# Kernel optimization log

Hardware: AMD Instinct MI355X
Metric: run time of the kernel (lower is better)

The kernel has to match this reference:

```python
import jax, jax.numpy as jnp
import numpy as np

S, B, C, H, E, V, T = 196, 64, 1024, 1024, 512, 32000, 20


def setup_inputs() -> dict:
    key = jax.random.key(0)
    ks = jax.random.split(key, 16)

    def w(k, shape, fan_in):
        return (jax.random.normal(k, shape, jnp.float32) / np.sqrt(fan_in)).astype(jnp.float32)

    emb_W = w(ks[2], (V, E), E).at[0].set(0.0)  # padding_idx=0
    return {
        'ctx': jax.random.normal(ks[0], (S, B, C), jnp.float32),
        'y': jax.random.randint(ks[1], (T, B), 0, V, jnp.int32),
        'emb_W': emb_W,
        'att_ctx2ctx': w(ks[3], (C, C), C),
        'att_hid2ctx': w(ks[4], (H, C), H),
        'att_mlp': w(ks[5], (C,), C),
        'gru_W_ih': w(ks[6], (3 * H, E + C), E + C),
        'gru_b_ih': jnp.zeros((3 * H,), jnp.float32),
        'gru_W_hh': w(ks[7], (3 * H, H), H),
        'gru_b_hh': jnp.zeros((3 * H,), jnp.float32),
        'hid2out_W': w(ks[8], (E, H), H),
        'hid2out_b': jnp.zeros((E,), jnp.float32),
        'out_ctx_W': w(ks[9], (E, C), C),
        'out_ctx_b': jnp.zeros((E,), jnp.float32),
        'out2prob_W': w(ks[10], (V, E), E),
        'out2prob_b': jnp.zeros((V,), jnp.float32),
    }


def reference(ctx, y, emb_W, att_ctx2ctx, att_hid2ctx, att_mlp,
              gru_W_ih, gru_b_ih, gru_W_hh, gru_b_hh,
              hid2out_W, hid2out_b, out_ctx_W, out_ctx_b,
              out2prob_W, out2prob_b):
    hidden = gru_W_hh.shape[1]
    y_emb = emb_W[y]                                        # [T, B, E]
    ctx_proj = jnp.einsum('sbc,cm->sbm', ctx, att_ctx2ctx)  # precompute ctx2ctx(ctx)

    def gru_cell(x, h):
        gi = x @ gru_W_ih.T + gru_b_ih
        gh = h @ gru_W_hh.T + gru_b_hh
        i_r, i_z, i_n = jnp.split(gi, 3, axis=-1)
        h_r, h_z, h_n = jnp.split(gh, 3, axis=-1)
        r = jax.nn.sigmoid(i_r + h_r)
        z = jax.nn.sigmoid(i_z + h_z)
        n = jnp.tanh(i_n + r * h_n)
        return (1.0 - z) * n + z * h

    def step(h, inp):
        y_t, tgt = inp                                      # [B,E], [B]
        # MLP attention over source positions S
        scores = jnp.einsum('sbm,m->sb', jnp.tanh(ctx_proj + (h @ att_hid2ctx)[None]), att_mlp)
        alpha = jax.nn.softmax(scores, axis=0)              # [S, B]
        z_t = jnp.einsum('sb,sbc->bc', alpha, ctx)          # [B, C]
        ht = gru_cell(jnp.concatenate([y_t, z_t], axis=-1), h)
        logit = jnp.tanh(ht @ hid2out_W.T + hid2out_b)      # hid2out (tanh FF)
        logit = logit + y_t                                 # prev2out
        logit = logit + z_t @ out_ctx_W.T + out_ctx_b       # ctx2out
        log_p = jax.nn.log_softmax(jnp.tanh(logit) @ out2prob_W.T + out2prob_b, axis=-1)
        mask = (tgt != 0).astype(log_p.dtype)               # NLLLoss ignore_index=0, sum
        nll = -jnp.sum(jnp.take_along_axis(log_p, tgt[:, None], axis=1)[:, 0] * mask)
        return ht, nll

    h0 = jnp.zeros((y.shape[1], hidden), ctx.dtype)         # dec_init='zero'
    _, nlls = jax.lax.scan(step, h0, (y_emb[:-1], y[1:]))
    return jnp.sum(nlls)
```

## Files before the change

kernel.cpp:

```cpp
#include <hip/hip_runtime.h>
#include <math.h>

#define TS_ 19

typedef float f32x4 __attribute__((ext_vector_type(4)));
typedef short s16x8 __attribute__((ext_vector_type(8)));
typedef unsigned short us;
typedef unsigned char uc;

__device__ __forceinline__ float sigmoidf_(float x) { return 1.f / (1.f + __expf(-x)); }

__device__ __forceinline__ float fast_tanh(float x) {
    float ax = fabsf(x);
    float e = __expf(-2.f * ax);
    float r = (1.f - e) * __builtin_amdgcn_rcpf(1.f + e);
    return copysignf(r, x);
}

__device__ __forceinline__ us f2b(float x) {
    union { float f; unsigned u; } v; v.f = x;
    unsigned r = v.u + 0x7fffu + ((v.u >> 16) & 1u);
    return (us)(r >> 16);
}
__device__ __forceinline__ float b2f(us u) {
    union { unsigned u; float f; } v; v.u = ((unsigned)u) << 16; return v.f;
}
__device__ __forceinline__ uc f2e4m3(float x) {
    return (uc)(__builtin_amdgcn_cvt_pk_fp8_f32(x, 0.f, 0, false) & 0xff);
}

#define MFMA(a, b, c) __builtin_amdgcn_mfma_f32_16x16x32_bf16((a), (b), (c), 0, 0, 0)
#define MFMA8(a, b, c) __builtin_amdgcn_mfma_f32_16x16x32_fp8_fp8((a), (b), (c), 0, 0, 0)

__device__ __forceinline__ f32x4 zero4() { return (f32x4){0.f, 0.f, 0.f, 0.f}; }

__device__ __forceinline__ f32x4 wg16(const us* ap, const us* bp, int nk, f32x4 acc) {
#pragma unroll 4
    for (int k = 0; k < nk; k += 32)
        acc = MFMA(*(const s16x8*)(ap + k), *(const s16x8*)(bp + k), acc);
    return acc;
}

__global__ __launch_bounds__(256) void k_cvt(const float* __restrict__ in,
                                             us* __restrict__ out, long n) {
    long i = ((long)blockIdx.x * 256 + threadIdx.x) * 4;
    long stride = (long)gridDim.x * 1024;
    for (; i < n; i += stride) {
        float4 v = *(const float4*)(in + i);
        ushort4 o = { f2b(v.x), f2b(v.y), f2b(v.z), f2b(v.w) };
        *(ushort4*)(out + i) = o;
    }
}

__global__ __launch_bounds__(256) void k_cvt8(const float* __restrict__ in,
                                              uc* __restrict__ out, long n) {
    long i = ((long)blockIdx.x * 256 + threadIdx.x) * 8;
    long stride = (long)gridDim.x * 2048;
    for (; i < n; i += stride) {
        float4 v0 = *(const float4*)(in + i);
        float4 v1 = *(const float4*)(in + i + 4);
        int lo = __builtin_amdgcn_cvt_pk_fp8_f32(v0.x, v0.y, 0, false);
        lo = __builtin_amdgcn_cvt_pk_fp8_f32(v0.z, v0.w, lo, true);
        int hi = __builtin_amdgcn_cvt_pk_fp8_f32(v1.x, v1.y, 0, false);
        hi = __builtin_amdgcn_cvt_pk_fp8_f32(v1.z, v1.w, hi, true);
        int2 o = { lo, hi };
        *(int2*)(out + i) = o;
    }
}

__global__ void k_tcvt(const float* __restrict__ in, us* __restrict__ out) {
    __shared__ float tile[32][33];
    int bx = blockIdx.x * 32, by = blockIdx.y * 32;
    int x = threadIdx.x, y0 = threadIdx.y;
    for (int yy = y0; yy < 32; yy += 8) tile[yy][x] = in[(by + yy) * 1024 + bx + x];
    __syncthreads();
    for (int yy = y0; yy < 32; yy += 8) out[(bx + yy) * 1024 + by + x] = f2b(tile[x][yy]);
}

__global__ __launch_bounds__(256) void k_yemb(const int* __restrict__ y,
                                              const float* __restrict__ embW,
                                              us* __restrict__ xc) {
    int t = blockIdx.x >> 6, b = blockIdx.x & 63;
    int row = y[t * 64 + b];
    const float* src = embW + (long)row * 512;
    us* dst = xc + (long)(t * 64 + b) * 2560;
    for (int e = threadIdx.x; e < 512; e += 256) dst[e] = f2b(src[e]);
}

__global__ __launch_bounds__(256) void k_prepw(const float* __restrict__ Wih,
                                               const float* __restrict__ Whh,
                                               us* __restrict__ Wg) {
    int n = blockIdx.x, tid = threadIdx.x;
    int cl = n >> 10;
    if (cl < 2) {
        long base = (long)n * 2560;
        const float* wi = Wih + (long)n * 1536;
        const float* wh = Whh + (long)n * 1024;
        for (int k = tid; k < 1536; k += 256) Wg[base + k] = f2b(wi[k]);
        for (int k = tid; k < 1024; k += 256) Wg[base + 1536 + k] = f2b(wh[k]);
    } else if (cl == 2) {
        long base = 5242880L + (long)(n - 2048) * 1536;
        const float* wi = Wih + (long)n * 1536;
        for (int k = tid; k < 1536; k += 256) Wg[base + k] = f2b(wi[k]);
    } else {
        long base = 6815744L + (long)(n - 3072) * 1024;
        const float* wh = Whh + (long)(n - 1024) * 1024;
        for (int k = tid; k < 1024; k += 256) Wg[base + k] = f2b(wh[k]);
    }
}

__global__ __launch_bounds__(512) void k_gemm(const us* __restrict__ A,
                                              const us* __restrict__ Bt,
                                              us* __restrict__ Cb) {
    int tid = threadIdx.x, lane = tid & 63, w = tid >> 6;
    int bm = blockIdx.x % 98, bn = blockIdx.x / 98;
    int mr = lane & 15, kb = lane >> 4;
    long m0 = (long)bm * 128 + (w >> 2) * 64;
    int n0 = bn * 256 + (w & 3) * 64;
    const us* ab = A + (m0 + mr) * 1024 + kb * 8;
    const us* bb = Bt + (long)(n0 + mr) * 1024 + kb * 8;

    f32x4 acc[4][4];
#pragma unroll
    for (int i = 0; i < 4; i++)
#pragma unroll
        for (int j = 0; j < 4; j++) acc[i][j] = zero4();

#pragma unroll 4
    for (int k0 = 0; k0 < 1024; k0 += 32) {
        s16x8 af[4], bf[4];
#pragma unroll
        for (int mt = 0; mt < 4; ++mt) af[mt] = *(const s16x8*)(ab + mt * 16384 + k0);
#pragma unroll
        for (int nt = 0; nt < 4; ++nt) bf[nt] = *(const s16x8*)(bb + nt * 16384 + k0);
#pragma unroll
        for (int mt = 0; mt < 4; ++mt)
#pragma unroll
            for (int nt = 0; nt < 4; ++nt)
                acc[mt][nt] = MFMA(af[mt], bf[nt], acc[mt][nt]);
    }
#pragma unroll
    for (int mt = 0; mt < 4; ++mt)
#pragma unroll
        for (int nt = 0; nt < 4; ++nt)
#pragma unroll
            for (int j = 0; j < 4; ++j)
                Cb[(m0 + mt * 16 + kb * 4 + j) * 1024 + n0 + nt * 16 + mr] =
                    f2b(acc[mt][nt][j]);
}

__global__ __launch_bounds__(256) void k_hproj(const us* __restrict__ hcur,
                                               const us* __restrict__ attbf,
                                               float* __restrict__ hpp) {
    int tid = threadIdx.x, lane = tid & 63, w = tid >> 6;
    int vn0 = (blockIdx.x >> 1) * 16, kc = blockIdx.x & 1;
    int m0 = w * 16, mr = lane & 15, kb = lane >> 4;
    const us* ap = hcur + (long)(m0 + mr) * 1024 + kc * 512 + kb * 8;
    const us* bp = attbf + (long)(vn0 + mr) * 1024 + kc * 512 + kb * 8;
    f32x4 acc = wg16(ap, bp, 512, zero4());
#pragma unroll
    for (int j = 0; j < 4; ++j)
        hpp[(long)kc * 65536 + (long)(m0 + kb * 4 + j) * 1024 + vn0 + mr] = acc[j];
}

__global__ __launch_bounds__(1024) void k_scores(const us* __restrict__ cpb,
                                                 const float* __restrict__ hpp,
                                                 const float* __restrict__ mlp,
                                                 float* __restrict__ scores) {
    __shared__ float hp[1024];
    __shared__ float ml[1024];
    int tid = threadIdx.x;
    int b = blockIdx.x >> 2, sq = blockIdx.x & 3;
    hp[tid] = hpp[(long)b * 1024 + tid] + hpp[65536 + (long)b * 1024 + tid];
    ml[tid] = mlp[tid];
    __syncthreads();
    int wv = tid >> 6, lane = tid & 63;
    int s0 = sq * 49;
    for (int s = s0 + wv; s < s0 + 49; s += 16) {
        const us* cp = cpb + (long)(s * 64 + b) * 1024 + lane * 16;
        s16x8 c0 = *(const s16x8*)cp;
        s16x8 c1 = *(const s16x8*)(cp + 8);
        int e0 = lane * 16;
        float acc = 0.f;
#pragma unroll
        for (int j = 0; j < 8; ++j)
            acc += fast_tanh(b2f((us)c0[j]) + hp[e0 + j]) * ml[e0 + j];
#pragma unroll
        for (int j = 0; j < 8; ++j)
            acc += fast_tanh(b2f((us)c1[j]) + hp[e0 + 8 + j]) * ml[e0 + 8 + j];
#pragma unroll
        for (int off = 32; off; off >>= 1) acc += __shfl_xor(acc, off, 64);
        if (lane == 0) scores[b * 196 + s] = acc;
    }
}

__global__ __launch_bounds__(512) void k_z(const float* __restrict__ scores,
                                           const us* __restrict__ ctxbf,
                                           us* __restrict__ xc, int t) {
    __shared__ float red[512];
    __shared__ float als[196];
    __shared__ float zp[256];
    int tid = threadIdx.x, b = blockIdx.x >> 2, ch = blockIdx.x & 3;
    const float* sc = scores + b * 196;
    float lm = (tid < 196) ? sc[tid] : -1e30f;
    red[tid] = lm; __syncthreads();
    for (int st = 256; st; st >>= 1) { if (tid < st) red[tid] = fmaxf(red[tid], red[tid + st]); __syncthreads(); }
    float m = red[0]; __syncthreads();
    float ls = (tid < 196) ? __expf(sc[tid] - m) : 0.f;
    red[tid] = ls; __syncthreads();
    for (int st = 256; st; st >>= 1) { if (tid < st) red[tid] += red[tid + st]; __syncthreads(); }
    float inv = 1.f / red[0];
    if (tid < 196) als[tid] = ls * inv;
    __syncthreads();
    int c = ch * 256 + (tid & 255);
    int sh = tid >> 8;
    const us* cp = ctxbf + (long)b * 1024 + c;
    float a0 = 0.f;
    int sb = sh * 98;
    for (int s = sb; s < sb + 98; s += 2) {
        a0 += als[s] * b2f(cp[(long)s * 65536]) +
              als[s + 1] * b2f(cp[(long)(s + 1) * 65536]);
    }
    if (sh) zp[tid & 255] = a0;
    __syncthreads();
    if (!sh) {
        a0 += zp[tid & 255];
        xc[(long)(t * 64 + b) * 2560 + 512 + c] = f2b(a0);
    }
}

__global__ __launch_bounds__(512) void k_gruh2(us* __restrict__ xc,
                                               const us* __restrict__ Wg,
                                               const float* __restrict__ bih,
                                               const float* __restrict__ bhh,
                                               float* __restrict__ hf32,
                                               us* __restrict__ ht_all, int t) {
    __shared__ float lg[2048];
    int tid = threadIdx.x, lane = tid & 63, w = tid >> 6;
    int mr = lane & 15, kb = lane >> 4;
    int g = w >> 1, kh = w & 1;
    int mq = blockIdx.x & 3, jt = blockIdx.x >> 2;
    int m0 = mq * 16, j0 = jt * 16;
    const us* xr = xc + (long)t * 163840 + (long)(m0 + mr) * 2560;

    f32x4 acc = zero4();
    if (g == 0) {
        acc = wg16(xr + kh * 1280 + kb * 8,
                   Wg + (long)(j0 + mr) * 2560 + kh * 1280 + kb * 8, 1280, acc);
    } else if (g == 1) {
        acc = wg16(xr + kh * 1280 + kb * 8,
                   Wg + (long)(1024 + j0 + mr) * 2560 + kh * 1280 + kb * 8, 1280, acc);
    } else if (g == 2) {
        acc = wg16(xr + kh * 768 + kb * 8,
                   Wg + 5242880L + (long)(j0 + mr) * 1536 + kh * 768 + kb * 8, 768, acc);
    } else {
        acc = wg16(xr + 1536 + kh * 512 + kb * 8,
                   Wg + 6815744L + (long)(j0 + mr) * 1024 + kh * 512 + kb * 8, 512, acc);
    }
#pragma unroll
    for (int j = 0; j < 4; ++j)
        lg[(g * 2 + kh) * 256 + (kb * 4 + j) * 16 + mr] = acc[j];
    __syncthreads();

    if (tid < 256) {
        int ml = tid >> 4, jj = tid & 15;
        int b = m0 + ml, j = j0 + jj;
        float gr = lg[0 * 256 + ml * 16 + jj] + lg[1 * 256 + ml * 16 + jj];
        float gz = lg[2 * 256 + ml * 16 + jj] + lg[3 * 256 + ml * 16 + jj];
        float gi = lg[4 * 256 + ml * 16 + jj] + lg[5 * 256 + ml * 16 + jj];
        float gh = lg[6 * 256 + ml * 16 + jj] + lg[7 * 256 + ml * 16 + jj];
        float r  = sigmoidf_(gr + bih[j] + bhh[j]);
        float zz = sigmoidf_(gz + bih[1024 + j] + bhh[1024 + j]);
        float n  = fast_tanh(gi + bih[2048 + j] + r * (gh + bhh[2048 + j]));
        float h = (1.f - zz) * n + zz * hf32[b * 1024 + j];
        hf32[b * 1024 + j] = h;
        us hb = f2b(h);
        ht_all[(long)((t + 1) * 64 + b) * 1024 + j] = hb;
        if (t < TS_ - 1) xc[(long)((t + 1) * 64 + b) * 2560 + 1536 + j] = hb;
    }
}

__global__ __launch_bounds__(256) void k_outb(const us* __restrict__ ht_all,
                                              const us* __restrict__ xc,
                                              const us* __restrict__ h2obf,
                                              const float* __restrict__ h2ob,
                                              const us* __restrict__ octxbf,
                                              const float* __restrict__ octxb,
                                              us* __restrict__ obf_all,
                                              uc* __restrict__ obf8) {
    int tid = threadIdx.x, lane = tid & 63, w = tid >> 6;
    int mr = lane & 15, kb = lane >> 4;
    int m0 = blockIdx.x * 64;
    int n0 = blockIdx.y * 256 + w * 64;
    f32x4 a1[4][4], a2[4][4];
#pragma unroll
    for (int i = 0; i < 4; i++)
#pragma unroll
        for (int j = 0; j < 4; j++) { a1[i][j] = zero4(); a2[i][j] = zero4(); }

    for (int k0 = 0; k0 < 1024; k0 += 32) {
        s16x8 bf[4], af[4];
#pragma unroll
        for (int nt = 0; nt < 4; ++nt)
            bf[nt] = *(const s16x8*)(h2obf + (long)(n0 + nt * 16 + mr) * 1024 + k0 + kb * 8);
#pragma unroll
        for (int mt = 0; mt < 4; ++mt)
            af[mt] = *(const s16x8*)(ht_all + (long)(64 + m0 + mt * 16 + mr) * 1024 + k0 + kb * 8);
#pragma unroll
        for (int mt = 0; mt < 4; ++mt)
#pragma unroll
            for (int nt = 0; nt < 4; ++nt)
                a1[mt][nt] = MFMA(af[mt], bf[nt], a1[mt][nt]);
    }
    for (int k0 = 0; k0 < 1024; k0 += 32) {
        s16x8 bf[4], af[4];
#pragma unroll
        for (int nt = 0; nt < 4; ++nt)
            bf[nt] = *(const s16x8*)(octxbf + (long)(n0 + nt * 16 + mr) * 1024 + k0 + kb * 8);
#pragma unroll
        for (int mt = 0; mt < 4; ++mt)
            af[mt] = *(const s16x8*)(xc + (long)(m0 + mt * 16 + mr) * 2560 + 512 + k0 + kb * 8);
#pragma unroll
        for (int mt = 0; mt < 4; ++mt)
#pragma unroll
            for (int nt = 0; nt < 4; ++nt)
                a2[mt][nt] = MFMA(af[mt], bf[nt], a2[mt][nt]);
    }
#pragma unroll
    for (int mt = 0; mt < 4; ++mt)
#pragma unroll
        for (int nt = 0; nt < 4; ++nt) {
            int e = n0 + nt * 16 + mr;
            float b1 = h2ob[e], b2 = octxb[e];
#pragma unroll
            for (int j = 0; j < 4; ++j) {
                long row = m0 + mt * 16 + kb * 4 + j;
                float ye = b2f(xc[row * 2560 + e]);
                float val = fast_tanh(fast_tanh(a1[mt][nt][j] + b1) + ye + a2[mt][nt][j] + b2);
                obf_all[(row << 9) + e] = f2b(val);
                obf8[(row << 9) + e] = f2e4m3(val);
            }
        }
}

__global__ __launch_bounds__(512) void k_vocab8(const uc* __restrict__ obf8,
                                                const uc* __restrict__ o2p8,
                                                const float* __restrict__ o2pb,
                                                float* __restrict__ pm,
                                                float* __restrict__ ps) {
    int tid = threadIdx.x, lane = tid & 63, w = tid >> 6;
    int mr = lane & 15, kb = lane >> 4;
    int x = blockIdx.x & 7, idx = blockIdx.x >> 3;
    int nb = x * 32 + idx / 5, mb = idx % 5;
    int wm = w >> 1, wn = w & 1;
    int n0 = nb * 128 + wn * 64;
    int m0 = mb * 256 + wm * 64;
    const long* ab = (const long*)(obf8 + (long)(m0 + mr) * 512 + kb * 8);
    const long* bb = (const long*)(o2p8 + (long)(n0 + mr) * 512 + kb * 8);
    f32x4 acc[4][4];
#pragma unroll
    for (int i = 0; i < 4; i++)
#pragma unroll
        for (int j = 0; j < 4; j++) acc[i][j] = zero4();

#pragma unroll 4
    for (int kq = 0; kq < 64; kq += 4) {
        long af[4], bf[4];
#pragma unroll
        for (int nt = 0; nt < 4; ++nt) bf[nt] = bb[nt * 1024 + kq];
#pragma unroll
        for (int mt = 0; mt < 4; ++mt) af[mt] = ab[mt * 1024 + kq];
#pragma unroll
        for (int mt = 0; mt < 4; ++mt)
#pragma unroll
            for (int nt = 0; nt < 4; ++nt)
                acc[mt][nt] = MFMA8(af[mt], bf[nt], acc[mt][nt]);
    }
    float bv[4];
#pragma unroll
    for (int nt = 0; nt < 4; ++nt) {
        int vn = n0 + nt * 16 + mr;
        bv[nt] = (vn < 32000) ? o2pb[vn] : -1e30f;
    }
#pragma unroll
    for (int mt = 0; mt < 4; ++mt)
#pragma unroll
        for (int j = 0; j < 4; ++j) {
            float x0 = acc[mt][0][j] + bv[0];
            float x1 = acc[mt][1][j] + bv[1];
            float x2 = acc[mt][2][j] + bv[2];
            float x3 = acc[mt][3][j] + bv[3];
            float m = fmaxf(fmaxf(x0, x1), fmaxf(x2, x3));
            float s = __expf(x0 - m) + __expf(x1 - m) + __expf(x2 - m) + __expf(x3 - m);
#pragma unroll
            for (int off = 1; off <= 8; off <<= 1) {
                float mo = __shfl_xor(m, off, 64), so = __shfl_xor(s, off, 64);
                float nm = fmaxf(m, mo);
                s = s * __expf(m - nm) + so * __expf(mo - nm);
                m = nm;
            }
            if (mr == 0) {
                int row = m0 + mt * 16 + kb * 4 + j;
                pm[(long)(nb * 2 + wn) * 1280 + row] = m;
                ps[(long)(nb * 2 + wn) * 1280 + row] = s;
            }
        }
}

__global__ __launch_bounds__(64) void k_lseb(const float* __restrict__ pm,
                                             const float* __restrict__ ps,
                                             const us* __restrict__ obf_all,
                                             const float* __restrict__ o2pW,
                                             const float* __restrict__ o2pb,
                                             const int* __restrict__ y,
                                             float* __restrict__ out) {
    int r = blockIdx.x, lane = threadIdx.x;
    int t = r >> 6, b = r & 63;
    int tgt = y[(t + 1) * 64 + b];
    float m = -1e30f, s = 0.f;
    for (int p = lane; p < 512; p += 64) {
        float mi = pm[(long)p * 1280 + r], si = ps[(long)p * 1280 + r];
        float nm = fmaxf(m, mi);
        s = s * __expf(m - nm) + si * __expf(mi - nm);
        m = nm;
    }
#pragma unroll
    for (int off = 32; off; off >>= 1) {
        float mo = __shfl_xor(m, off, 64), so = __shfl_xor(s, off, 64);
        float nm = fmaxf(m, mo);
        s = s * __expf(m - nm) + so * __expf(mo - nm);
        m = nm;
    }
    float d = 0.f;
    const float* wr = o2pW + (long)tgt * 512;
#pragma unroll
    for (int k = 0; k < 8; ++k)
        d += b2f(obf_all[(long)r * 512 + lane + k * 64]) * wr[lane + k * 64];
#pragma unroll
    for (int off = 32; off; off >>= 1) d += __shfl_xor(d, off, 64);
    if (lane == 0 && tgt != 0)
        atomicAdd(out, (m + __logf(s)) - (d + o2pb[tgt]));
}

extern "C" void kernel_launch(void* const* d_in, const int* in_sizes, int n_in,
                              void* d_out, int out_size, void* d_ws, size_t ws_size,
                              hipStream_t stream) {
    const float* ctx     = (const float*)d_in[0];
    const int*   y       = (const int*)d_in[1];
    const float* embW    = (const float*)d_in[2];
    const float* att_c2c = (const float*)d_in[3];
    const float* att_h2c = (const float*)d_in[4];
    const float* mlp     = (const float*)d_in[5];
    const float* Wih     = (const float*)d_in[6];
    const float* bih     = (const float*)d_in[7];
    const float* Whh     = (const float*)d_in[8];
    const float* bhh     = (const float*)d_in[9];
    const float* h2oW    = (const float*)d_in[10];
    const float* h2ob    = (const float*)d_in[11];
    const float* octxW   = (const float*)d_in[12];
    const float* octxb   = (const float*)d_in[13];
    const float* o2pW    = (const float*)d_in[14];
    const float* o2pb    = (const float*)d_in[15];
    float* out = (float*)d_out;

    char* base = (char*)d_ws;
    us* ctxbf   = (us*)base; base += 25690112L;
    us* cpbf    = (us*)base; base += 25690112L;
    us* c2cT    = (us*)base; base += 2097152L;
    us* attbf   = (us*)base; base += 2097152L;
    us* Wg      = (us*)base; base += 15728640L;
    us* h2obf   = (us*)base; base += 1048576L;
    us* octxbf  = (us*)base; base += 1048576L;
    uc* o2p8    = (uc*)base; base += 16777216L;
    us* xc      = (us*)base; base += 6225920L;
    us* ht_all  = (us*)base; base += 2621440L;
    us* obf_all = (us*)base; base += 1310720L;
    uc* obf8    = (uc*)base; base += 655360L;
    float* hf32   = (float*)base; base += 262144L;
    float* hpp    = (float*)base; base += 524288L;
    float* scb    = (float*)base; base += 50176L;
    float* pm   = (float*)cpbf;
    float* ps   = pm + 655360L;

    (void)hipMemsetAsync(d_out, 0, sizeof(float), stream);
    (void)hipMemsetAsync(hf32, 0, 262144, stream);
    (void)hipMemsetAsync(ht_all, 0, 131072, stream);
    (void)hipMemsetAsync(obf_all + 1216L * 512, 0, 65536, stream);
    (void)hipMemsetAsync(obf8 + 1216L * 512, 0, 32768, stream);
    (void)hipMemsetAsync(o2p8 + 16384000L, 0, 393216, stream);
    (void)hipMemsetAsync(xc, 0, 6225920, stream);

    k_yemb<<<TS_ * 64, 256, 0, stream>>>(y, embW, xc);
    k_tcvt<<<dim3(32, 32), dim3(32, 8), 0, stream>>>(att_c2c, c2cT);
    k_tcvt<<<dim3(32, 32), dim3(32, 8), 0, stream>>>(att_h2c, attbf);
    k_cvt<<<2048, 256, 0, stream>>>(ctx, ctxbf, 12845056L);
    k_cvt<<<512, 256, 0, stream>>>(h2oW, h2obf, 524288L);
    k_cvt<<<512, 256, 0, stream>>>(octxW, octxbf, 524288L);
    k_cvt8<<<2048, 256, 0, stream>>>(o2pW, o2p8, 16384000L);
    k_prepw<<<4096, 256, 0, stream>>>(Wih, Whh, Wg);
    k_gemm<<<392, 512, 0, stream>>>(ctxbf, c2cT, cpbf);

    for (int t = 0; t < TS_; t++) {
        k_hproj<<<128, 256, 0, stream>>>(ht_all + (long)t * 65536, attbf, hpp);
        k_scores<<<256, 1024, 0, stream>>>(cpbf, hpp, mlp, scb);
        k_z<<<256, 512, 0, stream>>>(scb, ctxbf, xc, t);
        k_gruh2<<<256, 512, 0, stream>>>(xc, Wg, bih, bhh, hf32, ht_all, t);
    }

    k_outb<<<dim3(19, 2), 256, 0, stream>>>(ht_all, xc, h2obf, h2ob, octxbf, octxb,
                                            obf_all, obf8);
    k_vocab8<<<1280, 512, 0, stream>>>(obf8, o2p8, o2pb, pm, ps);
    k_lseb<<<1216, 64, 0, stream>>>(pm, ps, obf_all, o2pW, o2pb, y, out);
}
```

Measured before the change: 1.163 ms.

## Stage GEMM and vocab tiles through swizzled LDS with direct global-to-LDS loads

```diff
diff --git a/kernel.cpp b/kernel.cpp
--- a/kernel.cpp
+++ b/kernel.cpp
@@ -39,6 +39,12 @@
     for (int k = 0; k < nk; k += 32)
         acc = MFMA(*(const s16x8*)(ap + k), *(const s16x8*)(bp + k), acc);
     return acc;
+}
+
+__device__ __forceinline__ void gload_lds16(const void* g, void* l) {
+    __builtin_amdgcn_global_load_lds(
+        (const __attribute__((address_space(1))) unsigned int*)g,
+        (__attribute__((address_space(3))) unsigned int*)l, 16, 0, 0);
 }
 
 __global__ __launch_bounds__(256) void k_cvt(const float* __restrict__ in,
@@ -109,16 +115,18 @@
     }
 }
 
-__global__ __launch_bounds__(512) void k_gemm(const us* __restrict__ A,
+__global__ __launch_bounds__(256) void k_gemm(const us* __restrict__ A,
                                               const us* __restrict__ Bt,
                                               us* __restrict__ Cb) {
+    __shared__ us As[8192], Bs[8192];
     int tid = threadIdx.x, lane = tid & 63, w = tid >> 6;
+    int mr = lane & 15, kb = lane >> 4;
     int bm = blockIdx.x % 98, bn = blockIdx.x / 98;
-    int mr = lane & 15, kb = lane >> 4;
-    long m0 = (long)bm * 128 + (w >> 2) * 64;
-    int n0 = bn * 256 + (w & 3) * 64;
-    const us* ab = A + (m0 + mr) * 1024 + kb * 8;
-    const us* bb = Bt + (long)(n0 + mr) * 1024 + kb * 8;
+    long m0 = (long)bm * 128;
+    int n0 = bn * 128;
+    int wr = w >> 1, wc = w & 1;
+    int srow = w * 32 + (lane >> 3);
+    int ib = (lane & 7) * 16;
 
     f32x4 acc[4][4];
 #pragma unroll
@@ -126,18 +134,36 @@
 #pragma unroll
         for (int j = 0; j < 4; j++) acc[i][j] = zero4();
 
-#pragma unroll 4
-    for (int k0 = 0; k0 < 1024; k0 += 32) {
-        s16x8 af[4], bf[4];
-#pragma unroll
-        for (int mt = 0; mt < 4; ++mt) af[mt] = *(const s16x8*)(ab + mt * 16384 + k0);
-#pragma unroll
-        for (int nt = 0; nt < 4; ++nt) bf[nt] = *(const s16x8*)(bb + nt * 16384 + k0);
-#pragma unroll
-        for (int mt = 0; mt < 4; ++mt)
-#pragma unroll
-            for (int nt = 0; nt < 4; ++nt)
-                acc[mt][nt] = MFMA(af[mt], bf[nt], acc[mt][nt]);
+    for (int kt = 0; kt < 16; ++kt) {
+        int k0 = kt * 64;
+        __syncthreads();
+#pragma unroll
+        for (int c = 0; c < 4; ++c) {
+            int r = srow + c * 8;
+            int sw = (ib ^ ((r & 7) << 4)) >> 1;
+            gload_lds16(A + (m0 + r) * 1024 + k0 + sw, &As[w * 2048 + c * 512]);
+            gload_lds16(Bt + (long)(n0 + r) * 1024 + k0 + sw, &Bs[w * 2048 + c * 512]);
+        }
+        __syncthreads();
+#pragma unroll
+        for (int ks = 0; ks < 2; ++ks) {
+            s16x8 af[4], bf[4];
+#pragma unroll
+            for (int mt = 0; mt < 4; ++mt) {
+                int r = wr * 64 + mt * 16 + mr;
+                af[mt] = *(const s16x8*)&As[(r * 128 + ((ks * 64 + kb * 16) ^ ((r & 7) << 4))) >> 1];
+            }
+#pragma unroll
+            for (int nt = 0; nt < 4; ++nt) {
+                int r = wc * 64 + nt * 16 + mr;
+                bf[nt] = *(const s16x8*)&Bs[(r * 128 + ((ks * 64 + kb * 16) ^ ((r & 7) << 4))) >> 1];
+            }
+#pragma unroll
+            for (int mt = 0; mt < 4; ++mt)
+#pragma unroll
+                for (int nt = 0; nt < 4; ++nt)
+                    acc[mt][nt] = MFMA(af[mt], bf[nt], acc[mt][nt]);
+        }
     }
 #pragma unroll
     for (int mt = 0; mt < 4; ++mt)
@@ -145,8 +171,8 @@
         for (int nt = 0; nt < 4; ++nt)
 #pragma unroll
             for (int j = 0; j < 4; ++j)
-                Cb[(m0 + mt * 16 + kb * 4 + j) * 1024 + n0 + nt * 16 + mr] =
-                    f2b(acc[mt][nt][j]);
+                Cb[(m0 + wr * 64 + mt * 16 + kb * 4 + j) * 1024 +
+                   n0 + wc * 64 + nt * 16 + mr] = f2b(acc[mt][nt][j]);
 }
 
 __global__ __launch_bounds__(256) void k_hproj(const us* __restrict__ hcur,
@@ -343,43 +369,64 @@
         }
 }
 
-__global__ __launch_bounds__(512) void k_vocab8(const uc* __restrict__ obf8,
+__global__ __launch_bounds__(256) void k_vocab8(const uc* __restrict__ obf8,
                                                 const uc* __restrict__ o2p8,
                                                 const float* __restrict__ o2pb,
                                                 float* __restrict__ pm,
                                                 float* __restrict__ ps) {
+    __shared__ uc As[8192], Bs[8192];
     int tid = threadIdx.x, lane = tid & 63, w = tid >> 6;
     int mr = lane & 15, kb = lane >> 4;
-    int x = blockIdx.x & 7, idx = blockIdx.x >> 3;
-    int nb = x * 32 + idx / 5, mb = idx % 5;
-    int wm = w >> 1, wn = w & 1;
-    int n0 = nb * 128 + wn * 64;
-    int m0 = mb * 256 + wm * 64;
-    const long* ab = (const long*)(obf8 + (long)(m0 + mr) * 512 + kb * 8);
-    const long* bb = (const long*)(o2p8 + (long)(n0 + mr) * 512 + kb * 8);
+    int xq = blockIdx.x & 7, idx = blockIdx.x >> 3;
+    int nb = xq * 32 + idx / 10, mb = idx % 10;
+    int m0 = mb * 128, n0 = nb * 128;
+    int wr = w >> 1, wc = w & 1;
+    int srow = w * 32 + (lane >> 2);
+    int ib = (lane & 3) * 16;
+
     f32x4 acc[4][4];
 #pragma unroll
     for (int i = 0; i < 4; i++)
 #pragma unroll
         for (int j = 0; j < 4; j++) acc[i][j] = zero4();
 
-#pragma unroll 4
-    for (int kq = 0; kq < 64; kq += 4) {
-        long af[4], bf[4];
-#pragma unroll
-        for (int nt = 0; nt < 4; ++nt) bf[nt] = bb[nt * 1024 + kq];
-#pragma unroll
-        for (int mt = 0; mt < 4; ++mt) af[mt] = ab[mt * 1024 + kq];
-#pragma unroll
-        for (int mt = 0; mt < 4; ++mt)
-#pragma unroll
-            for (int nt = 0; nt < 4; ++nt)
-                acc[mt][nt] = MFMA8(af[mt], bf[nt], acc[mt][nt]);
-    }
+    for (int kt = 0; kt < 8; ++kt) {
+        int k0 = kt * 64;
+        __syncthreads();
+#pragma unroll
+        for (int c = 0; c < 2; ++c) {
+            int r = srow + c * 16;
+            int sw = ib ^ ((r & 6) << 3);
+            gload_lds16(obf8 + (long)(m0 + r) * 512 + k0 + sw, &As[w * 2048 + c * 1024]);
+            gload_lds16(o2p8 + (long)(n0 + r) * 512 + k0 + sw, &Bs[w * 2048 + c * 1024]);
+        }
+        __syncthreads();
+#pragma unroll
+        for (int ks = 0; ks < 2; ++ks) {
+            long af[4], bf[4];
+#pragma unroll
+            for (int mt = 0; mt < 4; ++mt) {
+                int r = wr * 64 + mt * 16 + mr;
+                af[mt] = *(const long*)&As[r * 64 + ((ks * 32 + kb * 8) ^ ((r & 6) << 3))];
+            }
+#pragma unroll
+            for (int nt = 0; nt < 4; ++nt) {
+                int r = wc * 64 + nt * 16 + mr;
+                bf[nt] = *(const long*)&Bs[r * 64 + ((ks * 32 + kb * 8) ^ ((r & 6) << 3))];
+            }
+#pragma unroll
+            for (int mt = 0; mt < 4; ++mt)
+#pragma unroll
+                for (int nt = 0; nt < 4; ++nt)
+                    acc[mt][nt] = MFMA8(af[mt], bf[nt], acc[mt][nt]);
+        }
+    }
+
+    int n0w = n0 + wc * 64;
     float bv[4];
 #pragma unroll
     for (int nt = 0; nt < 4; ++nt) {
-        int vn = n0 + nt * 16 + mr;
+        int vn = n0w + nt * 16 + mr;
         bv[nt] = (vn < 32000) ? o2pb[vn] : -1e30f;
     }
 #pragma unroll
@@ -400,9 +447,9 @@
                 m = nm;
             }
             if (mr == 0) {
-                int row = m0 + mt * 16 + kb * 4 + j;
-                pm[(long)(nb * 2 + wn) * 1280 + row] = m;
-                ps[(long)(nb * 2 + wn) * 1280 + row] = s;
+                int row = m0 + wr * 64 + mt * 16 + kb * 4 + j;
+                pm[(long)(nb * 2 + wc) * 1280 + row] = m;
+                ps[(long)(nb * 2 + wc) * 1280 + row] = s;
             }
         }
 }
@@ -498,7 +545,7 @@
     k_cvt<<<512, 256, 0, stream>>>(octxW, octxbf, 524288L);
     k_cvt8<<<2048, 256, 0, stream>>>(o2pW, o2p8, 16384000L);
     k_prepw<<<4096, 256, 0, stream>>>(Wih, Whh, Wg);
-    k_gemm<<<392, 512, 0, stream>>>(ctxbf, c2cT, cpbf);
+    k_gemm<<<784, 256, 0, stream>>>(ctxbf, c2cT, cpbf);
 
     for (int t = 0; t < TS_; t++) {
         k_hproj<<<128, 256, 0, stream>>>(ht_all + (long)t * 65536, attbf, hpp);
@@ -509,6 +556,6 @@
 
     k_outb<<<dim3(19, 2), 256, 0, stream>>>(ht_all, xc, h2obf, h2ob, octxbf, octxb,
                                             obf_all, obf8);
-    k_vocab8<<<1280, 512, 0, stream>>>(obf8, o2p8, o2pb, pm, ps);
+    k_vocab8<<<2560, 256, 0, stream>>>(obf8, o2p8, o2pb, pm, ps);
     k_lseb<<<1216, 64, 0, stream>>>(pm, ps, obf_all, o2pW, o2pb, y, out);
 }
```

New measurement: 975.4 us. 16.1% less time.
